# Performance work log

Hardware: AMD Instinct MI355X
Metric: run time of the kernel (lower is better)

## Reference

```python
import jax, jax.numpy as jnp
import numpy as np

N_NODES, N_EDGES, N_REL, F_DIM, N_HEAD, N_LAYERS = 20000, 100000, 1000, 128, 4, 4
NEG_SLOPE = 0.2  # PyG GATv2Conv default negative_slope


def _gatv2_layer(x, ea_full, src, dst, Wl, bl, Wr, br, We, att, bias):
    # x: [N, F]; ea_full: [Etot, F] edge attrs (incl. self-loop rows)
    N = x.shape[0]
    H, C = att.shape  # heads, out-dim per head
    xl = (x @ Wl + bl).reshape(N, H, C)          # source-side projection
    xr = (x @ Wr + br).reshape(N, H, C)          # target-side projection
    ee = (ea_full @ We).reshape(-1, H, C)        # [Etot, H, C] edge embedding
    # GATv2 scoring: leaky_relu(x_i + x_j + e) . att
    e = jax.nn.leaky_relu(xl[src] + xr[dst] + ee, NEG_SLOPE)
    logits = jnp.einsum('ehc,hc->eh', e, att)    # [Etot, H]
    # segment softmax over edges grouped by destination node
    m = jax.ops.segment_max(logits, dst, num_segments=N)
    p = jnp.exp(logits - m[dst])
    denom = jax.ops.segment_sum(p, dst, num_segments=N)
    alpha = p / denom[dst]                       # [Etot, H]
    out = jax.ops.segment_sum(alpha[:, :, None] * xl[src], dst, num_segments=N)
    return out.mean(axis=1) + bias               # concat=False -> head mean


def setup_inputs() -> dict:
    key = jax.random.key(0)
    ks = jax.random.split(key, 12)
    N, E, R, F, H, L = N_NODES, N_EDGES, N_REL, F_DIM, N_HEAD, N_LAYERS
    HC = H * F
    s = 1.0 / np.sqrt(F)
    return {
        'x': jax.random.normal(ks[0], (N, F), jnp.float32),
        'edge_index': jax.random.randint(ks[1], (2, E), 0, N, dtype=jnp.int32),
        'relations': jax.random.normal(ks[2], (R, F), jnp.float32),
        'relation_index': jax.random.randint(ks[3], (E,), 0, R, dtype=jnp.int32),
        'Wl': jax.random.normal(ks[4], (L, F, HC), jnp.float32) * s,
        'bl': jnp.zeros((L, HC), jnp.float32),
        'Wr': jax.random.normal(ks[5], (L, F, HC), jnp.float32) * s,
        'br': jnp.zeros((L, HC), jnp.float32),
        'We': jax.random.normal(ks[6], (L, F, HC), jnp.float32) * s,
        'att': jax.random.normal(ks[7], (L, H, F), jnp.float32) * s,
        'bias': jnp.zeros((L, F), jnp.float32),
    }


def reference(x, edge_index, relations, relation_index, Wl, bl, Wr, br, We, att, bias):
    N = x.shape[0]
    sl = jnp.arange(N, dtype=edge_index.dtype)
    src = jnp.concatenate([edge_index[0], sl])   # add_self_loops=True
    dst = jnp.concatenate([edge_index[1], sl])
    ea = relations[relation_index]               # [E, F]
    # self-loop edge_attr uses fill_value='mean' (PyG default)
    ea_mean = ea.mean(axis=0)
    ea_full = jnp.concatenate([ea, jnp.broadcast_to(ea_mean, (N, ea.shape[1]))])
    h = x
    for l in range(N_LAYERS):
        h = _gatv2_layer(h, ea_full, src, dst, Wl[l], bl[l], Wr[l], br[l], We[l], att[l], bias[l])
    return (h, relations)
```

## Files before the change

kernel.cpp:

```cpp
#include <hip/hip_runtime.h>
#include <hip/hip_bf16.h>

#define N_NODES   20000
#define N_EDGES   100000
#define N_REL     1000
#define F_DIM     128
#define N_HEAD    4
#define HC        512
#define HC2       256
#define N_LAYERS  4
#define REL_EXT_ROWS 1008
#define NEG_SLOPE 0.2f
#define PROJ_NODE_X 157

typedef __attribute__((ext_vector_type(8))) short short8;
typedef __attribute__((ext_vector_type(4))) float floatx4;

__device__ __forceinline__ float loadIn(const void* p, size_t i, int f32) {
    if (f32) return ((const float*)p)[i];
    union { unsigned int u; float f; } c;
    c.u = ((unsigned int)((const unsigned short*)p)[i]) << 16;
    return c.f;
}

__device__ __forceinline__ unsigned short f2bf(float v) {
    __hip_bfloat16 b = __float2bfloat16(v);
    return *(unsigned short*)&b;
}

__device__ __forceinline__ void unpack2(unsigned int u, float& lo, float& hi) {
    union { unsigned int u; float f; } a, b;
    a.u = u << 16;
    b.u = u & 0xFFFF0000u;
    lo = a.f; hi = b.f;
}

__device__ __forceinline__ void unpack8(uint4 v, float* f) {
    unpack2(v.x, f[0], f[1]);
    unpack2(v.y, f[2], f[3]);
    unpack2(v.z, f[4], f[5]);
    unpack2(v.w, f[6], f[7]);
}

__global__ void detect_kernel(const unsigned short* __restrict__ x, int* __restrict__ flag) {
    int t = threadIdx.x;
    int cnt = 0;
    for (int j = t; j < 256; j += 64) {
        int e = (x[j] >> 7) & 0xFF;
        if (e >= 143) cnt++;
    }
    for (int off = 32; off; off >>= 1) cnt += __shfl_xor(cnt, off);
    if (t == 0) flag[0] = (cnt >= 8) ? 1 : 0;
}


__global__ void hist_kernel(const int* __restrict__ dst, const int* __restrict__ rel,
                            int* __restrict__ deg, int* __restrict__ rcount) {
    int e = blockIdx.x * 256 + threadIdx.x;
    if (e < N_EDGES) {
        atomicAdd(&deg[dst[e]], 1);
        atomicAdd(&rcount[rel[e]], 1);
    }
}

__global__ void ea_mean_kernel(const int* __restrict__ rcount,
                               const void* __restrict__ relations,
                               float* __restrict__ ea_mean, const int* __restrict__ flag) {
    int f32 = flag[0];
    int b = blockIdx.x;
    int t = threadIdx.x;
    int col = t & 127;
    int rhalf = t >> 7;
    float acc = 0.f;
    for (int j = 0; j < 4; ++j) {
        int r = b * 8 + j * 2 + rhalf;
        acc += (float)rcount[r] * loadIn(relations, (size_t)r * F_DIM + col, f32);
    }
    __shared__ float part[256];
    part[t] = acc;
    __syncthreads();
    if (t < 128)
        atomicAdd(&ea_mean[col], (part[t] + part[t + 128]) * (1.f / (float)N_EDGES));
}

__global__ void relext_kernel(const void* __restrict__ relations,
                              const float* __restrict__ ea_mean,
                              unsigned short* __restrict__ rel_ext, const int* __restrict__ flag) {
    int idx = blockIdx.x * 256 + threadIdx.x;
    if (idx >= REL_EXT_ROWS * F_DIM) return;
    int f32 = flag[0];
    int r = idx >> 7;
    int c = idx & 127;
    float v;
    if (r < N_REL)       v = loadIn(relations, idx, f32);
    else if (r == N_REL) v = ea_mean[c];
    else                 v = 0.f;
    rel_ext[idx] = f2bf(v);
}

__global__ void scan_kernel(const int* __restrict__ deg,
                            int* __restrict__ row_start, int* __restrict__ cursor) {
    __shared__ int part[1024];
    int t = threadIdx.x;
    const int CH = (N_NODES + 1023) / 1024;
    int base = t * CH;
    int sum = 0;
    for (int j = 0; j < CH; ++j) {
        int idx = base + j;
        if (idx < N_NODES) sum += deg[idx];
    }
    part[t] = sum;
    __syncthreads();
    for (int off = 1; off < 1024; off <<= 1) {
        int u = (t >= off) ? part[t - off] : 0;
        __syncthreads();
        part[t] += u;
        __syncthreads();
    }
    int run = part[t] - sum;
    for (int j = 0; j < CH; ++j) {
        int idx = base + j;
        if (idx < N_NODES) {
            row_start[idx] = run;
            cursor[idx] = run;
            run += deg[idx];
        }
    }
    if (t == 1023) row_start[N_NODES] = part[1023];
}

__global__ void scatter_kernel(const int* __restrict__ src, const int* __restrict__ dst,
                               const int* __restrict__ rel, int* __restrict__ cursor,
                               int* __restrict__ csr_pack) {
    int e = blockIdx.x * 256 + threadIdx.x;
    if (e < N_EDGES) {
        int d = dst[e];
        int p = atomicAdd(&cursor[d], 1);
        csr_pack[p] = src[e] | (rel[e] << 16);
    }
}

__global__ void build8_kernel(const int* __restrict__ row_start,
                              const int* __restrict__ csr_pack,
                              int* __restrict__ csr8) {
    int i = blockIdx.x * 256 + threadIdx.x;
    if (i >= N_NODES) return;
    int rs = row_start[i];
    int deg = row_start[i + 1] - rs;
    if (deg < 0) deg = 0;
    int dcap = deg > 4095 ? 4095 : deg;
    csr8[i * 8] = rs | (dcap << 17);
    #pragma unroll
    for (int k = 0; k < 7; ++k)
        csr8[i * 8 + 1 + k] = (k < deg) ? csr_pack[rs + k] : 0;
}

__global__ void tail_kernel(const void* __restrict__ relations, void* __restrict__ out,
                            const int* __restrict__ flag) {
    int i = blockIdx.x * 256 + threadIdx.x;
    if (i >= N_REL * F_DIM) return;
    int f32 = flag[0];
    float v = loadIn(relations, i, f32);
    size_t o = (size_t)N_NODES * F_DIM + i;
    if (f32) ((float*)out)[o] = v;
    else     ((unsigned short*)out)[o] = f2bf(v);
}

__global__ void w_transpose_kernel(const void* __restrict__ Wl, const void* __restrict__ Wr,
                                   const void* __restrict__ We,
                                   unsigned short* __restrict__ Wt, const int* __restrict__ flag) {
    int f32 = flag[0];
    int k0 = blockIdx.x * 64;
    int n0 = blockIdx.y * 64;
    int mat = blockIdx.z;
    const void* src = (mat < 4) ? Wl : (mat < 8 ? Wr : We);
    size_t base = (size_t)(mat & 3) * F_DIM * HC;
    unsigned short* dst = Wt + (size_t)mat * HC * F_DIM;
    __shared__ float T[64][65];
    int t = threadIdx.x;
    int r = t >> 2, cq = t & 3;
    for (int j = 0; j < 16; ++j) {
        int n = cq * 16 + j;
        T[n][r] = loadIn(src, base + (size_t)(k0 + r) * HC + n0 + n, f32);
    }
    __syncthreads();
    for (int j = 0; j < 16; ++j) {
        int k = cq * 16 + j;
        dst[(size_t)(n0 + r) * F_DIM + k0 + k] = f2bf(T[r][k]);
    }
}

__launch_bounds__(256, 3)
__global__ void proj_kernel(const void* __restrict__ A_node, int a_input,
                            const unsigned short* __restrict__ rel_ext,
                            const unsigned short* __restrict__ Wlt,
                            const unsigned short* __restrict__ Wrt,
                            const unsigned short* __restrict__ Wet,
                            const void* __restrict__ bl, const void* __restrict__ br,
                            size_t boff,
                            unsigned short* __restrict__ xl,
                            unsigned short* __restrict__ xr,
                            unsigned short* __restrict__ re,
                            const int* __restrict__ flag) {
    __shared__ __align__(16) short As[64][136];
    __shared__ __align__(16) short Cs[64 * 136];
    int f32 = flag[0];
    int t = threadIdx.x;
    int y = blockIdx.y;
    int isNode = (blockIdx.x < PROJ_NODE_X);

    const void* A;
    const unsigned short* Wt;
    const void* bias;
    unsigned short* out;
    int M, mbase, nT, a_f32;
    int n0 = (y & 3) * 128;
    if (isNode) {
        A = A_node; M = N_NODES; nT = 2;
        mbase = blockIdx.x * 128;
        a_f32 = a_input ? f32 : 0;
        if (y < 4) { Wt = Wlt; bias = bl; out = xl; }
        else       { Wt = Wrt; bias = br; out = xr; }
    } else {
        A = (const void*)rel_ext; M = REL_EXT_ROWS; nT = 4;
        int rowchunk = (blockIdx.x - PROJ_NODE_X) * 2 + (y >> 2);
        mbase = rowchunk * 256;
        a_f32 = 0;
        Wt = Wet; bias = nullptr; out = re;
    }

    int wave = t >> 6, lane = t & 63;
    int wm = (wave >> 1) * 32, wn = (wave & 1) * 64;
    int r16 = lane & 15, quad = lane >> 4;

    short8 breg[2][2][4];
    #pragma unroll
    for (int half = 0; half < 2; ++half)
        #pragma unroll
        for (int kk = 0; kk < 2; ++kk)
            #pragma unroll
            for (int ni = 0; ni < 4; ++ni)
                breg[half][kk][ni] = *(const short8*)(
                    Wt + (size_t)(n0 + wn + ni * 16 + r16) * F_DIM + half * 64 + kk * 32 + quad * 8);

    float bv[4];
    #pragma unroll
    for (int ni = 0; ni < 4; ++ni)
        bv[ni] = bias ? loadIn(bias, boff + n0 + wn + ni * 16 + r16, f32) : 0.f;

    int sRow = 0, sCol = 0;

    short8 aS[4];
    #pragma unroll
    for (int j = 0; j < 4; ++j) {
        int c = t + j * 256;
        int row = c >> 4;
        int colc = (c & 15) * 8;
        int gm = mbase + row;
        short8 v = (short8){0, 0, 0, 0, 0, 0, 0, 0};
        if (gm < M) {
            size_t idx = (size_t)gm * F_DIM + colc;
            if (a_f32) {
                const float* Af = (const float*)A;
                for (int q = 0; q < 8; ++q) v[q] = (short)f2bf(Af[idx + q]);
            } else {
                v = *(const short8*)((const unsigned short*)A + idx);
            }
        }
        aS[j] = v;
    }
    (void)sRow; (void)sCol;

    for (int ct = 0; ct < nT; ++ct) {
        int m0 = mbase + ct * 64;
        __syncthreads();
        #pragma unroll
        for (int j = 0; j < 4; ++j) {
            int c = t + j * 256;
            *(short8*)&As[c >> 4][(c & 15) * 8] = aS[j];
        }
        short8 aN[4];
        if (ct + 1 < nT) {
            int mb = mbase + (ct + 1) * 64;
            #pragma unroll
            for (int j = 0; j < 4; ++j) {
                int c = t + j * 256;
                int row = c >> 4;
                int colc = (c & 15) * 8;
                int gm = mb + row;
                short8 v = (short8){0, 0, 0, 0, 0, 0, 0, 0};
                if (gm < M) {
                    size_t idx = (size_t)gm * F_DIM + colc;
                    if (a_f32) {
                        const float* Af = (const float*)A;
                        for (int q = 0; q < 8; ++q) v[q] = (short)f2bf(Af[idx + q]);
                    } else {
                        v = *(const short8*)((const unsigned short*)A + idx);
                    }
                }
                aN[j] = v;
            }
            #pragma unroll
            for (int j = 0; j < 4; ++j) aS[j] = aN[j];
        }
        __syncthreads();

        floatx4 acc[2][4];
        #pragma unroll
        for (int mi = 0; mi < 2; ++mi)
            #pragma unroll
            for (int ni = 0; ni < 4; ++ni)
                acc[mi][ni] = (floatx4){0.f, 0.f, 0.f, 0.f};

        #pragma unroll
        for (int half = 0; half < 2; ++half) {
            #pragma unroll
            for (int kk = 0; kk < 2; ++kk) {
                short8 a[2];
                #pragma unroll
                for (int mi = 0; mi < 2; ++mi)
                    a[mi] = *(const short8*)&As[wm + mi * 16 + r16][half * 64 + kk * 32 + quad * 8];
                #pragma unroll
                for (int mi = 0; mi < 2; ++mi)
                    #pragma unroll
                    for (int ni = 0; ni < 4; ++ni)
                        acc[mi][ni] = __builtin_amdgcn_mfma_f32_16x16x32_bf16(
                            a[mi], breg[half][kk][ni], acc[mi][ni], 0, 0, 0);
            }
        }

        #pragma unroll
        for (int mi = 0; mi < 2; ++mi) {
            #pragma unroll
            for (int ni = 0; ni < 4; ++ni) {
                int col = wn + ni * 16 + r16;
                #pragma unroll
                for (int r = 0; r < 4; ++r) {
                    int rowl = wm + mi * 16 + quad * 4 + r;
                    Cs[rowl * 136 + col] = (short)f2bf(acc[mi][ni][r] + bv[ni]);
                }
            }
        }
        __syncthreads();
        #pragma unroll
        for (int j = 0; j < 4; ++j) {
            int c = t + j * 256;
            int rowl = c >> 4;
            int colc = (c & 15) * 8;
            int gm = m0 + rowl;
            if (gm < M)
                *(short8*)(out + (size_t)gm * HC + n0 + colc) =
                    *(const short8*)&Cs[rowl * 136 + colc];
        }
    }
}

__launch_bounds__(128)
__global__ void edge_kernel(const unsigned int* __restrict__ xl2,
                            const unsigned int* __restrict__ xr2,
                            const unsigned int* __restrict__ re2,
                            const int* __restrict__ csr8,
                            const int* __restrict__ csr_pack,
                            const void* __restrict__ att, size_t att_off,
                            const void* __restrict__ bias, size_t bias_off,
                            void* __restrict__ hout, int final_layer,
                            const int* __restrict__ flag) {
    int f32 = flag[0];
    int wid = threadIdx.x >> 6;
    int lane = threadIdx.x & 63;
    int i = blockIdx.x * 2 + wid;
    if (i >= N_NODES) return;
    int h = lane >> 4;
    int q = lane & 15;
    int loff = h * 64 + q * 4;

    uint4 h0 = *(const uint4*)(csr8 + (size_t)i * 8);
    uint4 h1 = *(const uint4*)(csr8 + (size_t)i * 8 + 4);
    int rs  = (int)(h0.x & 0x1FFFF);
    int deg = (int)(h0.x >> 17) & 0xFFF;
    int ew[7] = { (int)h0.y, (int)h0.z, (int)h0.w, (int)h1.x, (int)h1.y, (int)h1.z, (int)h1.w };

    float xr[8];
    { uint4 v = *(const uint4*)(xr2 + (size_t)i * HC2 + loff); unpack8(v, xr); }
    float er[8];
    { uint4 v = *(const uint4*)(re2 + (size_t)N_REL * HC2 + loff); unpack8(v, er); }
    float av[8];
    #pragma unroll
    for (int j = 0; j < 8; ++j)
        av[j] = loadIn(att, att_off + (size_t)h * F_DIM + q * 8 + j, f32);

    int nIn = deg > 7 ? 7 : deg;
    uint4 xv[7], rv[7];
    #pragma unroll
    for (int k = 0; k < 7; ++k) {
        if (k < nIn) {
            int pk = ew[k];
            int sn = pk & 0xFFFF;        if (sn >= N_NODES) sn = 0;
            int rn = (pk >> 16) & 0x3FF; if (rn > N_REL) rn = N_REL;
            xv[k] = *(const uint4*)(xl2 + (size_t)sn * HC2 + loff);
            rv[k] = *(const uint4*)(re2 + (size_t)rn * HC2 + loff);
        }
    }

    float acc[8];
    float s;
    {
        float xs[8];
        uint4 v = *(const uint4*)(xl2 + (size_t)i * HC2 + loff);
        unpack8(v, xs);
        float part = 0.f;
        #pragma unroll
        for (int j = 0; j < 8; ++j) {
            float u = xs[j] + xr[j] + er[j];
            u = fmaxf(u, NEG_SLOPE * u);
            part = fmaf(u, av[j], part);
        }
        #pragma unroll
        for (int off = 8; off; off >>= 1) part += __shfl_xor(part, off);
        part = fminf(fmaxf(part, -60.f), 60.f);
        float p = __expf(part);
        s = p;
        #pragma unroll
        for (int j = 0; j < 8; ++j) acc[j] = p * xs[j];
    }

    #pragma unroll
    for (int k = 0; k < 7; ++k) {
        if (k < nIn) {
            float xlv[8], ee[8];
            unpack8(xv[k], xlv);
            unpack8(rv[k], ee);
            float part = 0.f;
            #pragma unroll
            for (int j = 0; j < 8; ++j) {
                float u = xlv[j] + xr[j] + ee[j];
                u = fmaxf(u, NEG_SLOPE * u);
                part = fmaf(u, av[j], part);
            }
            #pragma unroll
            for (int off = 8; off; off >>= 1) part += __shfl_xor(part, off);
            part = fminf(fmaxf(part, -60.f), 60.f);
            float pp = __expf(part);
            s += pp;
            #pragma unroll
            for (int j = 0; j < 8; ++j) acc[j] = fmaf(pp, xlv[j], acc[j]);
        }
    }

    if (deg > 7) {
        int e1 = rs + deg;
        if (e1 > N_EDGES) e1 = N_EDGES;
        for (int b = rs + 7; b < e1; b += 4) {
            int nb = e1 - b; if (nb > 4) nb = 4;
            uint4 xo[4], ro[4];
            #pragma unroll
            for (int k = 0; k < 4; ++k) {
                if (k < nb) {
                    int pk = csr_pack[b + k];
                    int sn = pk & 0xFFFF;        if (sn >= N_NODES) sn = 0;
                    int rn = (pk >> 16) & 0x3FF; if (rn > N_REL) rn = N_REL;
                    xo[k] = *(const uint4*)(xl2 + (size_t)sn * HC2 + loff);
                    ro[k] = *(const uint4*)(re2 + (size_t)rn * HC2 + loff);
                }
            }
            #pragma unroll
            for (int k = 0; k < 4; ++k) {
                if (k < nb) {
                    float xlv[8], ee[8];
                    unpack8(xo[k], xlv);
                    unpack8(ro[k], ee);
                    float part = 0.f;
                    #pragma unroll
                    for (int j = 0; j < 8; ++j) {
                        float u = xlv[j] + xr[j] + ee[j];
                        u = fmaxf(u, NEG_SLOPE * u);
                        part = fmaf(u, av[j], part);
                    }
                    #pragma unroll
                    for (int off = 8; off; off >>= 1) part += __shfl_xor(part, off);
                    part = fminf(fmaxf(part, -60.f), 60.f);
                    float pp = __expf(part);
                    s += pp;
                    #pragma unroll
                    for (int j = 0; j < 8; ++j) acc[j] = fmaf(pp, xlv[j], acc[j]);
                }
            }
        }
    }

    float inv = 1.f / s;
    float outv[8];
    #pragma unroll
    for (int j = 0; j < 8; ++j) outv[j] = acc[j] * inv;
    #pragma unroll
    for (int j = 0; j < 8; ++j) {
        outv[j] += __shfl_xor(outv[j], 16);
        outv[j] += __shfl_xor(outv[j], 32);
    }

    if (h == 0) {
        float bv[8];
        #pragma unroll
        for (int j = 0; j < 8; ++j)
            bv[j] = loadIn(bias, bias_off + q * 8 + j, f32);
        size_t o = (size_t)i * F_DIM + q * 8;
        if (final_layer && f32) {
            float* op = (float*)hout + o;
            float4 lo, hi;
            lo.x = outv[0] * 0.25f + bv[0];
            lo.y = outv[1] * 0.25f + bv[1];
            lo.z = outv[2] * 0.25f + bv[2];
            lo.w = outv[3] * 0.25f + bv[3];
            hi.x = outv[4] * 0.25f + bv[4];
            hi.y = outv[5] * 0.25f + bv[5];
            hi.z = outv[6] * 0.25f + bv[6];
            hi.w = outv[7] * 0.25f + bv[7];
            *(float4*)op = lo;
            *(float4*)(op + 4) = hi;
        } else {
            unsigned int w[4];
            #pragma unroll
            for (int p = 0; p < 4; ++p) {
                float v0 = outv[2 * p] * 0.25f + bv[2 * p];
                float v1 = outv[2 * p + 1] * 0.25f + bv[2 * p + 1];
                w[p] = (unsigned int)f2bf(v0) | ((unsigned int)f2bf(v1) << 16);
            }
            *(uint4*)((unsigned short*)hout + o) = *(uint4*)w;
        }
    }
}


extern "C" void kernel_launch(void* const* d_in, const int* in_sizes, int n_in,
                              void* d_out, int out_size, void* d_ws, size_t ws_size,
                              hipStream_t stream) {
    const void* x          = d_in[0];
    const int*  edge_index = (const int*)d_in[1];
    const void* relations  = d_in[2];
    const int*  rel_index  = (const int*)d_in[3];
    const void* Wl         = d_in[4];
    const void* bl         = d_in[5];
    const void* Wr         = d_in[6];
    const void* br         = d_in[7];
    const void* We         = d_in[8];
    const void* att        = d_in[9];
    const void* bias       = d_in[10];

    char* ws = (char*)d_ws;
    size_t off = 0;
    auto alloc = [&](size_t bytes) -> void* {
        void* p = ws + off;
        off = (off + bytes + 255) & ~(size_t)255;
        return p;
    };
    int*            flag     = (int*)alloc(4);
    char*           zero0    = ws + off;
    int*            deg      = (int*)alloc(N_NODES * 4);
    int*            rcount   = (int*)alloc(N_REL * 4);
    float*          ea_mean  = (float*)alloc(F_DIM * 4);
    size_t          zlen     = (size_t)((ws + off) - zero0);
    int*            row_start= (int*)alloc((N_NODES + 1) * 4);
    int*            cursor   = (int*)alloc(N_NODES * 4);
    int*            csr_pack = (int*)alloc(N_EDGES * 4);
    int*            csr8     = (int*)alloc((size_t)N_NODES * 8 * 4);
    unsigned short* rel_ext  = (unsigned short*)alloc((size_t)REL_EXT_ROWS * F_DIM * 2);
    unsigned short* Wt       = (unsigned short*)alloc((size_t)12 * HC * F_DIM * 2);
    unsigned short* re       = (unsigned short*)alloc((size_t)REL_EXT_ROWS * HC * 2);
    unsigned short* hbuf     = (unsigned short*)alloc((size_t)N_NODES * F_DIM * 2);
    unsigned short* xl       = (unsigned short*)alloc((size_t)N_NODES * HC * 2);
    unsigned short* xr       = (unsigned short*)alloc((size_t)N_NODES * HC * 2);

    const int* esrc = edge_index;
    const int* edst = edge_index + N_EDGES;

    detect_kernel<<<1, 64, 0, stream>>>((const unsigned short*)x, flag);
    hipMemsetAsync(zero0, 0, zlen, stream);
    hist_kernel<<<(N_EDGES + 255) / 256, 256, 0, stream>>>(edst, rel_index, deg, rcount);
    ea_mean_kernel<<<N_REL / 8, 256, 0, stream>>>(rcount, relations, ea_mean, flag);
    relext_kernel<<<(REL_EXT_ROWS * F_DIM + 255) / 256, 256, 0, stream>>>(relations, ea_mean, rel_ext, flag);
    scan_kernel<<<1, 1024, 0, stream>>>(deg, row_start, cursor);
    scatter_kernel<<<(N_EDGES + 255) / 256, 256, 0, stream>>>(esrc, edst, rel_index, cursor, csr_pack);
    build8_kernel<<<(N_NODES + 255) / 256, 256, 0, stream>>>(row_start, csr_pack, csr8);
    w_transpose_kernel<<<dim3(2, 8, 12), 256, 0, stream>>>(Wl, Wr, We, Wt, flag);
    tail_kernel<<<(N_REL * F_DIM + 255) / 256, 256, 0, stream>>>(relations, d_out, flag);

    const void* hin = x;
    int a_input = 1;
    for (int l = 0; l < N_LAYERS; ++l) {
        const unsigned short* Wlt = Wt + (size_t)l * HC * F_DIM;
        const unsigned short* Wrt = Wt + (size_t)(4 + l) * HC * F_DIM;
        const unsigned short* Wet = Wt + (size_t)(8 + l) * HC * F_DIM;
        proj_kernel<<<dim3(PROJ_NODE_X + 2, 8), 256, 0, stream>>>(
            hin, a_input, rel_ext, Wlt, Wrt, Wet,
            bl, br, (size_t)l * HC,
            xl, xr, re, flag);
        int final_layer = (l == N_LAYERS - 1);
        void* hout = final_layer ? d_out : (void*)hbuf;
        edge_kernel<<<(N_NODES + 1) / 2, 128, 0, stream>>>(
            (const unsigned int*)xl, (const unsigned int*)xr, (const unsigned int*)re,
            csr8, csr_pack,
            att, (size_t)l * N_HEAD * F_DIM,
            bias, (size_t)l * F_DIM,
            hout, final_layer, flag);
        hin = hbuf;
        a_input = 0;
    }
}
```

Baseline: 423.7 us.

## Double-buffer proj A tiles via async global-to-LDS loads with XOR swizzle

```diff
diff --git a/kernel.cpp b/kernel.cpp
--- a/kernel.cpp
+++ b/kernel.cpp
@@ -11,7 +11,7 @@
 #define N_LAYERS  4
 #define REL_EXT_ROWS 1008
 #define NEG_SLOPE 0.2f
-#define PROJ_NODE_X 157
+#define PROJ_NODE_X 79
 
 typedef __attribute__((ext_vector_type(8))) short short8;
 typedef __attribute__((ext_vector_type(4))) float floatx4;
@@ -40,6 +40,13 @@
     unpack2(v.y, f[2], f[3]);
     unpack2(v.z, f[4], f[5]);
     unpack2(v.w, f[6], f[7]);
+}
+
+__device__ __forceinline__ void gload_lds16(const unsigned short* g, short* l) {
+    __builtin_amdgcn_global_load_lds(
+        (const __attribute__((address_space(1))) unsigned int*)g,
+        (__attribute__((address_space(3))) unsigned int*)l,
+        16, 0, 0);
 }
 
 __global__ void detect_kernel(const unsigned short* __restrict__ x, int* __restrict__ flag) {
@@ -51,6 +58,22 @@
     }
     for (int off = 32; off; off >>= 1) cnt += __shfl_xor(cnt, off);
     if (t == 0) flag[0] = (cnt >= 8) ? 1 : 0;
+}
+
+__global__ void xcast_kernel(const void* __restrict__ x, unsigned short* __restrict__ xbf,
+                             const int* __restrict__ flag) {
+    int idx = blockIdx.x * 256 + threadIdx.x;
+    if (idx >= N_NODES * F_DIM / 4) return;
+    int f32 = flag[0];
+    uint2 o;
+    if (f32) {
+        float4 v = ((const float4*)x)[idx];
+        o.x = (unsigned int)f2bf(v.x) | ((unsigned int)f2bf(v.y) << 16);
+        o.y = (unsigned int)f2bf(v.z) | ((unsigned int)f2bf(v.w) << 16);
+    } else {
+        o = ((const uint2*)x)[idx];
+    }
+    ((uint2*)xbf)[idx] = o;
 }
 
 
@@ -191,7 +214,7 @@
 }
 
 __launch_bounds__(256, 3)
-__global__ void proj_kernel(const void* __restrict__ A_node, int a_input,
+__global__ void proj_kernel(const unsigned short* __restrict__ A_node,
                             const unsigned short* __restrict__ rel_ext,
                             const unsigned short* __restrict__ Wlt,
                             const unsigned short* __restrict__ Wrt,
@@ -202,32 +225,31 @@
                             unsigned short* __restrict__ xr,
                             unsigned short* __restrict__ re,
                             const int* __restrict__ flag) {
-    __shared__ __align__(16) short As[64][136];
+    __shared__ __align__(16) short As[2][64 * 128];
     __shared__ __align__(16) short Cs[64 * 136];
     int f32 = flag[0];
     int t = threadIdx.x;
     int y = blockIdx.y;
     int isNode = (blockIdx.x < PROJ_NODE_X);
 
-    const void* A;
+    const unsigned short* A;
     const unsigned short* Wt;
     const void* bias;
     unsigned short* out;
-    int M, mbase, nT, a_f32;
+    int M, mbase;
     int n0 = (y & 3) * 128;
     if (isNode) {
-        A = A_node; M = N_NODES; nT = 2;
-        mbase = blockIdx.x * 128;
-        a_f32 = a_input ? f32 : 0;
+        A = A_node; M = N_NODES;
+        mbase = blockIdx.x * 256;
         if (y < 4) { Wt = Wlt; bias = bl; out = xl; }
         else       { Wt = Wrt; bias = br; out = xr; }
     } else {
-        A = (const void*)rel_ext; M = REL_EXT_ROWS; nT = 4;
+        A = rel_ext; M = REL_EXT_ROWS;
         int rowchunk = (blockIdx.x - PROJ_NODE_X) * 2 + (y >> 2);
         mbase = rowchunk * 256;
-        a_f32 = 0;
         Wt = Wet; bias = nullptr; out = re;
     }
+    const int nT = 4;
 
     int wave = t >> 6, lane = t & 63;
     int wm = (wave >> 1) * 32, wn = (wave & 1) * 64;
@@ -248,62 +270,29 @@
     for (int ni = 0; ni < 4; ++ni)
         bv[ni] = bias ? loadIn(bias, boff + n0 + wn + ni * 16 + r16, f32) : 0.f;
 
-    int sRow = 0, sCol = 0;
-
-    short8 aS[4];
-    #pragma unroll
-    for (int j = 0; j < 4; ++j) {
-        int c = t + j * 256;
-        int row = c >> 4;
-        int colc = (c & 15) * 8;
-        int gm = mbase + row;
-        short8 v = (short8){0, 0, 0, 0, 0, 0, 0, 0};
-        if (gm < M) {
-            size_t idx = (size_t)gm * F_DIM + colc;
-            if (a_f32) {
-                const float* Af = (const float*)A;
-                for (int q = 0; q < 8; ++q) v[q] = (short)f2bf(Af[idx + q]);
-            } else {
-                v = *(const short8*)((const unsigned short*)A + idx);
-            }
-        }
-        aS[j] = v;
-    }
-    (void)sRow; (void)sCol;
-
+    auto STAGE = [&](int buf, int ct2) {
+        int base = mbase + ct2 * 64;
+        #pragma unroll
+        for (int j = 0; j < 4; ++j) {
+            int c = t + j * 256;
+            int row = c >> 4, ch = c & 15;
+            int gm = base + row;
+            if (gm >= M) gm = M - 1;
+            int sch = ch ^ (row & 15);
+            gload_lds16(A + (size_t)gm * F_DIM + sch * 8, &As[buf][c * 8]);
+        }
+    };
+
+    STAGE(0, 0);
+    asm volatile("s_waitcnt vmcnt(0)" ::: "memory");
+    __builtin_amdgcn_sched_barrier(0);
+    __syncthreads();
+
+    int cur = 0;
     for (int ct = 0; ct < nT; ++ct) {
         int m0 = mbase + ct * 64;
-        __syncthreads();
-        #pragma unroll
-        for (int j = 0; j < 4; ++j) {
-            int c = t + j * 256;
-            *(short8*)&As[c >> 4][(c & 15) * 8] = aS[j];
-        }
-        short8 aN[4];
-        if (ct + 1 < nT) {
-            int mb = mbase + (ct + 1) * 64;
-            #pragma unroll
-            for (int j = 0; j < 4; ++j) {
-                int c = t + j * 256;
-                int row = c >> 4;
-                int colc = (c & 15) * 8;
-                int gm = mb + row;
-                short8 v = (short8){0, 0, 0, 0, 0, 0, 0, 0};
-                if (gm < M) {
-                    size_t idx = (size_t)gm * F_DIM + colc;
-                    if (a_f32) {
-                        const float* Af = (const float*)A;
-                        for (int q = 0; q < 8; ++q) v[q] = (short)f2bf(Af[idx + q]);
-                    } else {
-                        v = *(const short8*)((const unsigned short*)A + idx);
-                    }
-                }
-                aN[j] = v;
-            }
-            #pragma unroll
-            for (int j = 0; j < 4; ++j) aS[j] = aN[j];
-        }
-        __syncthreads();
+        if (ct + 1 < nT) STAGE(cur ^ 1, ct + 1);
+        __builtin_amdgcn_sched_barrier(0);
 
         floatx4 acc[2][4];
         #pragma unroll
@@ -318,8 +307,11 @@
             for (int kk = 0; kk < 2; ++kk) {
                 short8 a[2];
                 #pragma unroll
-                for (int mi = 0; mi < 2; ++mi)
-                    a[mi] = *(const short8*)&As[wm + mi * 16 + r16][half * 64 + kk * 32 + quad * 8];
+                for (int mi = 0; mi < 2; ++mi) {
+                    int row = wm + mi * 16 + r16;
+                    int pch = (half * 8 + kk * 4 + quad) ^ (row & 15);
+                    a[mi] = *(const short8*)&As[cur][row * 128 + pch * 8];
+                }
                 #pragma unroll
                 for (int mi = 0; mi < 2; ++mi)
                     #pragma unroll
@@ -341,17 +333,25 @@
                 }
             }
         }
-        __syncthreads();
+        asm volatile("s_waitcnt lgkmcnt(0)" ::: "memory");
+        __builtin_amdgcn_s_barrier();
+
         #pragma unroll
         for (int j = 0; j < 4; ++j) {
             int c = t + j * 256;
             int rowl = c >> 4;
             int colc = (c & 15) * 8;
             int gm = m0 + rowl;
-            if (gm < M)
-                *(short8*)(out + (size_t)gm * HC + n0 + colc) =
-                    *(const short8*)&Cs[rowl * 136 + colc];
-        }
+            if (gm >= M) gm = M - 1;
+            *(short8*)(out + (size_t)gm * HC + n0 + colc) =
+                *(const short8*)&Cs[rowl * 136 + colc];
+        }
+        if (ct + 1 < nT) {
+            asm volatile("s_waitcnt vmcnt(4)" ::: "memory");
+            __builtin_amdgcn_sched_barrier(0);
+        }
+        __builtin_amdgcn_s_barrier();
+        cur ^= 1;
     }
 }
 
@@ -564,6 +564,7 @@
     int*            csr_pack = (int*)alloc(N_EDGES * 4);
     int*            csr8     = (int*)alloc((size_t)N_NODES * 8 * 4);
     unsigned short* rel_ext  = (unsigned short*)alloc((size_t)REL_EXT_ROWS * F_DIM * 2);
+    unsigned short* xbf      = (unsigned short*)alloc((size_t)N_NODES * F_DIM * 2);
     unsigned short* Wt       = (unsigned short*)alloc((size_t)12 * HC * F_DIM * 2);
     unsigned short* re       = (unsigned short*)alloc((size_t)REL_EXT_ROWS * HC * 2);
     unsigned short* hbuf     = (unsigned short*)alloc((size_t)N_NODES * F_DIM * 2);
@@ -575,6 +576,7 @@
 
     detect_kernel<<<1, 64, 0, stream>>>((const unsigned short*)x, flag);
     hipMemsetAsync(zero0, 0, zlen, stream);
+    xcast_kernel<<<(N_NODES * F_DIM / 4 + 255) / 256, 256, 0, stream>>>(x, xbf, flag);
     hist_kernel<<<(N_EDGES + 255) / 256, 256, 0, stream>>>(edst, rel_index, deg, rcount);
     ea_mean_kernel<<<N_REL / 8, 256, 0, stream>>>(rcount, relations, ea_mean, flag);
     relext_kernel<<<(REL_EXT_ROWS * F_DIM + 255) / 256, 256, 0, stream>>>(relations, ea_mean, rel_ext, flag);
@@ -584,14 +586,13 @@
     w_transpose_kernel<<<dim3(2, 8, 12), 256, 0, stream>>>(Wl, Wr, We, Wt, flag);
     tail_kernel<<<(N_REL * F_DIM + 255) / 256, 256, 0, stream>>>(relations, d_out, flag);
 
-    const void* hin = x;
-    int a_input = 1;
+    const unsigned short* hin = xbf;
     for (int l = 0; l < N_LAYERS; ++l) {
         const unsigned short* Wlt = Wt + (size_t)l * HC * F_DIM;
         const unsigned short* Wrt = Wt + (size_t)(4 + l) * HC * F_DIM;
         const unsigned short* Wet = Wt + (size_t)(8 + l) * HC * F_DIM;
         proj_kernel<<<dim3(PROJ_NODE_X + 2, 8), 256, 0, stream>>>(
-            hin, a_input, rel_ext, Wlt, Wrt, Wet,
+            hin, rel_ext, Wlt, Wrt, Wet,
             bl, br, (size_t)l * HC,
             xl, xr, re, flag);
         int final_layer = (l == N_LAYERS - 1);
@@ -603,6 +604,5 @@
             bias, (size_t)l * F_DIM,
             hout, final_layer, flag);
         hin = hbuf;
-        a_input = 0;
-    }
-}
+    }
+}
```

Result: faster. 405.4 us (-4.3%).
